# Performance work log

Hardware: AMD Instinct MI355X
Metric: run time of the kernel (lower is better)

Reference implementation:

```python
import jax, jax.numpy as jnp
import numpy as np

NSTEPS = 4
STEPSIZE = 1.0
B, N_PATCHES, D_LAT = 4, 81920, 32
HIDDEN, D_DYN = 128, 16


def setup_inputs() -> dict:
    key = jax.random.key(0)
    k1, k2, k3, k4 = jax.random.split(key, 4)
    z_old = jax.random.normal(k1, (B, N_PATCHES, D_LAT), dtype=jnp.float32)
    neighbour_list = jax.random.randint(k2, (N_PATCHES, 3), 0, N_PATCHES, dtype=jnp.int32)
    W1 = jax.random.normal(k3, (4 * D_LAT, HIDDEN), dtype=jnp.float32) * (1.0 / np.sqrt(4 * D_LAT))
    b1 = jnp.zeros((HIDDEN,), dtype=jnp.float32)
    W2 = jax.random.normal(k4, (HIDDEN, D_DYN), dtype=jnp.float32) * (1.0 / np.sqrt(HIDDEN))
    b2 = jnp.zeros((D_DYN,), dtype=jnp.float32)
    return {"z_old": z_old, "neighbour_list": neighbour_list, "W1": W1, "b1": b1, "W2": W2, "b2": b2}


def _step(z, neighbour_list, W1, b1, W2, b2):
    # gather neighbour features: (B, n_patches, 3, d_lat)
    neigh = z[:, neighbour_list, :]
    # z_mid: (B, n_patches, d_lat, 4) with slot 0 = self, slots 1..3 = neighbours
    z_mid = jnp.concatenate([z[..., None], jnp.swapaxes(neigh, -1, -2)], axis=-1)
    flat = z_mid.reshape(z.shape[0], z.shape[1], -1)  # (B, n_patches, 4*d_lat)
    h = jnp.tanh(flat @ W1 + b1)
    F_theta = h @ W2 + b2  # (B, n_patches, d_dyn)
    return z.at[:, :, :F_theta.shape[-1]].add(STEPSIZE * F_theta)


def reference(z_old, neighbour_list, W1, b1, W2, b2):
    z = z_old
    for _ in range(NSTEPS):
        z = _step(z, neighbour_list, W1, b1, W2, b2)
    return z
```

## Files before the change

### kernel.cpp

```cpp
#include <hip/hip_runtime.h>
#include <hip/hip_bf16.h>

typedef unsigned short u16;
typedef unsigned int u32;
typedef __attribute__((ext_vector_type(8))) short bf16x8;
typedef __attribute__((ext_vector_type(4))) float f32x4;
typedef __attribute__((ext_vector_type(4))) u16 u16x4;

#define NPATCH 81920
#define NBATCH 4
#define NROWS (NBATCH * NPATCH)
#define HID 128
#define CHUNK 64
#define NCHUNK (NROWS / CHUNK)
#define CPB (NPATCH / CHUNK)
#define GSTRIDE 512

__device__ __forceinline__ u16 f2bf(float x) {
  union { __hip_bfloat16 b; u16 u; } c; c.b = __float2bfloat16(x); return c.u;
}
__device__ __forceinline__ float bf2f(u16 h) {
  union { __hip_bfloat16 b; u16 u; } c; c.u = h; return __bfloat162float(c.b);
}

#define GLD(g, l) __builtin_amdgcn_global_load_lds( \
    (const __attribute__((address_space(1))) void*)(g), \
    (__attribute__((address_space(3))) void*)(l), 16, 0, 0)
#define SBAR() __builtin_amdgcn_s_barrier()
#define SCHED0() __builtin_amdgcn_sched_barrier(0)

__global__ void prep_w(const float* __restrict__ W1, const float* __restrict__ W2,
                       u16* __restrict__ wf, u16* __restrict__ w2f) {
  int t = blockIdx.x * 256 + threadIdx.x;
  if (t < 128 * 128) {
    int kp = t >> 7, n = t & 127;
    int s = kp >> 5, d = kp & 31;
    float v = W1[(d * 4 + s) * HID + n];
    u16 h = f2bf(v);
    u16 l = f2bf(v - bf2f(h));
    int kg = kp >> 3, j = kp & 7;
    int o = (kg * 128 + n) * 8 + j;
    wf[o] = h;
    wf[16384 + o] = l;
  } else if (t < 128 * 128 + 2048) {
    int u = t - 128 * 128;
    int k = u >> 4, o = u & 15;
    float v = W2[k * 16 + o];
    u16 h = f2bf(v);
    u16 l = f2bf(v - bf2f(h));
    int kt = k >> 5, lg = (k >> 3) & 3, j = k & 7;
    int idx = ((kt * 4 + lg) * 16 + o) * 8 + j;
    w2f[idx] = h;
    w2f[2048 + idx] = l;
  }
}

template<int MERGED>
__global__ void prep_z(const float* __restrict__ z, u16* __restrict__ A0, u16* __restrict__ B0) {
  int t = blockIdx.x * 256 + threadIdx.x;
  if (t >= NROWS * 8) return;
  size_t row = (size_t)(t >> 3);
  int q = t & 7;
  float4 v = *(const float4*)&z[row * 32 + q * 4];
  u16 h0 = f2bf(v.x), h1 = f2bf(v.y), h2 = f2bf(v.z), h3 = f2bf(v.w);
  u16 l0 = f2bf(v.x - bf2f(h0)), l1 = f2bf(v.y - bf2f(h1));
  u16 l2 = f2bf(v.z - bf2f(h2)), l3 = f2bf(v.w - bf2f(h3));
  u16x4 hh = {h0, h1, h2, h3};
  u16x4 ll = {l0, l1, l2, l3};
  int dd = (q & 3) * 4;
  if (MERGED) {
    int reg = (q < 4) ? 0 : 32;
    *(u16x4*)&A0[row * 64 + reg + dd] = hh;
    *(u16x4*)&A0[row * 64 + reg + 16 + dd] = ll;
    *(u16x4*)&B0[row * 64 + reg + dd] = hh;
    *(u16x4*)&B0[row * 64 + reg + 16 + dd] = ll;
  } else {
    u16* buf = (q < 4) ? A0 : B0;
    *(u16x4*)&buf[row * 32 + dd] = hh;
    *(u16x4*)&buf[row * 32 + 16 + dd] = ll;
  }
}

template<int FIRST, int LAST, int MERGED>
__global__ __launch_bounds__(256, 2) void step_kernel(
    const u16* __restrict__ Zin, u16* __restrict__ Zout,
    const u16* __restrict__ Sst,
    const float* __restrict__ zold, float* __restrict__ zf,
    const int* __restrict__ nl, const float* __restrict__ b1,
    const float* __restrict__ b2, const u16* __restrict__ wf,
    const u16* __restrict__ w2f) {
  __shared__ __align__(16) u16 AH[2][16 * 64 * 8];
  __shared__ __align__(16) u16 AL[2][16 * 64 * 8];
  __shared__ __align__(16) u16 W2H[2048];
  __shared__ __align__(16) u16 W2L[2048];

  const int tid = threadIdx.x;
  const int lane = tid & 63;
  const int w = tid >> 6;
  const int li = lane & 15;
  const int lg = lane >> 4;

  #pragma unroll
  for (int c = 0; c < 2; ++c) {
    int idx = tid + c * 256;
    int part = idx >> 8, slot = idx & 255;
    u16* dst = part ? W2L : W2H;
    *(bf16x8*)&dst[slot * 8] = *(const bf16x8*)&w2f[part * 2048 + slot * 8];
  }

  bf16x8 WH[2][4], WL[2][4];
  #pragma unroll
  for (int nt = 0; nt < 2; ++nt)
    #pragma unroll
    for (int kt = 0; kt < 4; ++kt) {
      int kg = kt * 4 + lg;
      int n = w * 32 + nt * 16 + li;
      WH[nt][kt] = *(const bf16x8*)&wf[(kg * 128 + n) * 8];
      WL[nt][kt] = *(const bf16x8*)&wf[16384 + (kg * 128 + n) * 8];
    }

  float b1v[2][4];
  #pragma unroll
  for (int nt = 0; nt < 2; ++nt)
    #pragma unroll
    for (int r = 0; r < 4; ++r)
      b1v[nt][r] = b1[w * 32 + nt * 16 + lg * 4 + r];
  float b2v = b2[li];

  #define NVLOAD(CN) nl[(((CN) * CHUNK - ((CN) / CPB) * NPATCH) + lane) * 3 + (w - 1)]

  #define STAGE(BUF, CN, NV) do {                                          \
    int b_ = (CN) / CPB;                                                   \
    int pb_ = (CN) * CHUNK - b_ * NPATCH;                                  \
    int ps_ = w ? (NV) : (pb_ + lane);                                     \
    size_t r_ = (size_t)b_ * NPATCH + (size_t)ps_;                         \
    u16* ah_ = &AH[BUF][(w * 4) * 512];                                    \
    u16* al_ = &AL[BUF][(w * 4) * 512];                                    \
    if (MERGED) {                                                          \
      const u16* s_ = Zin + r_ * 64;                                       \
      GLD(s_ + 0,  ah_ + 0);    GLD(s_ + 8,  ah_ + 512);                   \
      GLD(s_ + 32, ah_ + 1024); GLD(s_ + 40, ah_ + 1536);                  \
      GLD(s_ + 16, al_ + 0);    GLD(s_ + 24, al_ + 512);                   \
      GLD(s_ + 48, al_ + 1024); GLD(s_ + 56, al_ + 1536);                  \
    } else {                                                               \
      const u16* d_ = Zin + r_ * 32;                                       \
      const u16* t_ = Sst + r_ * 32;                                       \
      GLD(d_ + 0,  ah_ + 0);    GLD(d_ + 8,  ah_ + 512);                   \
      GLD(t_ + 0,  ah_ + 1024); GLD(t_ + 8,  ah_ + 1536);                  \
      GLD(d_ + 16, al_ + 0);    GLD(d_ + 24, al_ + 512);                   \
      GLD(t_ + 16, al_ + 1024); GLD(t_ + 24, al_ + 1536);                  \
    }                                                                      \
  } while (0)

  int c0 = blockIdx.x;
  int nv = 0, nv1 = 0;
  if (w) nv = NVLOAD(c0);
  {
    int c1 = c0 + GSTRIDE; if (c1 > NCHUNK - 1) c1 = NCHUNK - 1;
    if (w) nv1 = NVLOAD(c1);
  }
  STAGE(0, c0, nv);
  asm volatile("s_waitcnt lgkmcnt(0)" ::: "memory");
  int cur = 0;

  for (int c = c0; c < NCHUNK; c += GSTRIDE) {
    int cn = c + GSTRIDE;
    bool hn = cn < NCHUNK;
    if (hn) STAGE(cur ^ 1, cn, nv1);
    {
      int cnn = cn + GSTRIDE; if (cnn > NCHUNK - 1) cnn = NCHUNK - 1;
      if (w && hn) nv1 = NVLOAD(cnn);
    }
    if (!hn)        { asm volatile("s_waitcnt vmcnt(0)" ::: "memory"); }
    else if (w == 0){ asm volatile("s_waitcnt vmcnt(8)" ::: "memory"); }
    else            { asm volatile("s_waitcnt vmcnt(9)" ::: "memory"); }
    SCHED0(); SBAR(); SCHED0();

    f32x4 acc[2][4];
    #pragma unroll
    for (int nt = 0; nt < 2; ++nt)
      #pragma unroll
      for (int mt = 0; mt < 4; ++mt)
        acc[nt][mt] = (f32x4){0.f, 0.f, 0.f, 0.f};

    #pragma unroll
    for (int kt = 0; kt < 4; ++kt) {
      #pragma unroll
      for (int mt = 0; mt < 4; ++mt) {
        int off = ((kt * 4 + lg) * 64 + mt * 16 + li) * 8;
        bf16x8 ah = *(const bf16x8*)&AH[cur][off];
        bf16x8 al = *(const bf16x8*)&AL[cur][off];
        #pragma unroll
        for (int nt = 0; nt < 2; ++nt) {
          acc[nt][mt] = __builtin_amdgcn_mfma_f32_16x16x32_bf16(WH[nt][kt], ah, acc[nt][mt], 0, 0, 0);
          acc[nt][mt] = __builtin_amdgcn_mfma_f32_16x16x32_bf16(WH[nt][kt], al, acc[nt][mt], 0, 0, 0);
          acc[nt][mt] = __builtin_amdgcn_mfma_f32_16x16x32_bf16(WL[nt][kt], ah, acc[nt][mt], 0, 0, 0);
        }
      }
    }
    SCHED0(); SBAR(); SCHED0();

    #pragma unroll
    for (int nt = 0; nt < 2; ++nt) {
      #pragma unroll
      for (int mt = 0; mt < 4; ++mt) {
        u16 hh[4], ll[4];
        #pragma unroll
        for (int r = 0; r < 4; ++r) {
          float hval = acc[nt][mt][r] + b1v[nt][r];
          float e = __expf(2.0f * hval);
          float t = 1.0f - 2.0f / (e + 1.0f);
          hh[r] = f2bf(t);
          ll[r] = f2bf(t - bf2f(hh[r]));
        }
        int base = ((w * 4 + nt * 2 + (lg >> 1)) * 64 + mt * 16 + li) * 8 + (lg & 1) * 4;
        u16x4 hv = {hh[0], hh[1], hh[2], hh[3]};
        u16x4 lv = {ll[0], ll[1], ll[2], ll[3]};
        *(u16x4*)&AH[cur][base] = hv;
        *(u16x4*)&AL[cur][base] = lv;
      }
    }
    asm volatile("s_waitcnt lgkmcnt(0)" ::: "memory");
    SCHED0(); SBAR(); SCHED0();

    f32x4 acc2 = (f32x4){0.f, 0.f, 0.f, 0.f};
    #pragma unroll
    for (int kt = 0; kt < 4; ++kt) {
      int woff = ((kt * 4 + lg) * 16 + li) * 8;
      bf16x8 wh = *(const bf16x8*)&W2H[woff];
      bf16x8 wl = *(const bf16x8*)&W2L[woff];
      int off = ((kt * 4 + lg) * 64 + w * 16 + li) * 8;
      bf16x8 hh = *(const bf16x8*)&AH[cur][off];
      bf16x8 hl = *(const bf16x8*)&AL[cur][off];
      acc2 = __builtin_amdgcn_mfma_f32_16x16x32_bf16(hh, wh, acc2, 0, 0, 0);
      acc2 = __builtin_amdgcn_mfma_f32_16x16x32_bf16(hl, wh, acc2, 0, 0, 0);
      acc2 = __builtin_amdgcn_mfma_f32_16x16x32_bf16(hh, wl, acc2, 0, 0, 0);
    }

    #pragma unroll
    for (int r = 0; r < 4; ++r) {
      int rowg = c * CHUNK + w * 16 + lg * 4 + r;
      float F = acc2[r] + b2v;
      float zi = FIRST ? zold[(size_t)rowg * 32 + li] : zf[(size_t)rowg * 32 + li];
      float v = zi + F;
      zf[(size_t)rowg * 32 + li] = v;
      if (LAST) {
        zf[(size_t)rowg * 32 + 16 + li] = zold[(size_t)rowg * 32 + 16 + li];
      } else {
        u16 h = f2bf(v);
        u16 l = f2bf(v - bf2f(h));
        if (MERGED) {
          Zout[(size_t)rowg * 64 + li] = h;
          Zout[(size_t)rowg * 64 + 16 + li] = l;
        } else {
          Zout[(size_t)rowg * 32 + li] = h;
          Zout[(size_t)rowg * 32 + 16 + li] = l;
        }
      }
    }
    cur ^= 1;
  }
  #undef STAGE
  #undef NVLOAD
}

extern "C" void kernel_launch(void* const* d_in, const int* in_sizes, int n_in,
                              void* d_out, int out_size, void* d_ws, size_t ws_size,
                              hipStream_t stream) {
  const float* z_old = (const float*)d_in[0];
  const int* nl = (const int*)d_in[1];
  const float* W1 = (const float*)d_in[2];
  const float* b1 = (const float*)d_in[3];
  const float* W2 = (const float*)d_in[4];
  const float* b2 = (const float*)d_in[5];
  float* out = (float*)d_out;

  const size_t wOff = 73728;
  const size_t DbM = (size_t)NROWS * 64 * sizeof(u16);
  const size_t DbS = (size_t)NROWS * 32 * sizeof(u16);
  const size_t needM = wOff + 2 * DbM;
  u16* wf = (u16*)d_ws;
  u16* w2f = wf + 32768;
  char* base = (char*)d_ws + wOff;

  prep_w<<<72, 256, 0, stream>>>(W1, W2, wf, w2f);

  if (ws_size >= needM) {
    u16* ZA = (u16*)base;
    u16* ZB = (u16*)(base + DbM);
    prep_z<1><<<(NROWS * 8) / 256, 256, 0, stream>>>(z_old, ZA, ZB);
    step_kernel<1, 0, 1><<<GSTRIDE, 256, 0, stream>>>(ZA, ZB, nullptr, z_old, out, nl, b1, b2, wf, w2f);
    step_kernel<0, 0, 1><<<GSTRIDE, 256, 0, stream>>>(ZB, ZA, nullptr, z_old, out, nl, b1, b2, wf, w2f);
    step_kernel<0, 0, 1><<<GSTRIDE, 256, 0, stream>>>(ZA, ZB, nullptr, z_old, out, nl, b1, b2, wf, w2f);
    step_kernel<0, 1, 1><<<GSTRIDE, 256, 0, stream>>>(ZB, ZA, nullptr, z_old, out, nl, b1, b2, wf, w2f);
  } else {
    u16* S  = (u16*)base;
    u16* DA = (u16*)(base + DbS);
    u16* DB = (u16*)(base + 2 * DbS);
    prep_z<0><<<(NROWS * 8) / 256, 256, 0, stream>>>(z_old, DA, S);
    step_kernel<1, 0, 0><<<GSTRIDE, 256, 0, stream>>>(DA, DB, S, z_old, out, nl, b1, b2, wf, w2f);
    step_kernel<0, 0, 0><<<GSTRIDE, 256, 0, stream>>>(DB, DA, S, z_old, out, nl, b1, b2, wf, w2f);
    step_kernel<0, 0, 0><<<GSTRIDE, 256, 0, stream>>>(DA, DB, S, z_old, out, nl, b1, b2, wf, w2f);
    step_kernel<0, 1, 0><<<GSTRIDE, 256, 0, stream>>>(DB, DA, S, z_old, out, nl, b1, b2, wf, w2f);
  }
}
```

Before: 362.3 us.

## Restructure step kernel to per-wave 32-row tiles with register-held activations

Each wave now independently processes 32 rows, gathering neighbour rows directly into registers instead of staging them through LDS with global_load_lds and block barriers. W1 (hi/lo bf16 split) is cached in LDS and read per MFMA, while the hidden activations are moved between MFMA layouts with ds_bpermute instead of an LDS round trip. Stores and the residual load become 16-byte vectorised, and the tanh division becomes a hardware reciprocal. This removes block-level syncs, but it adds register pressure (acc[8][2], prefetched A fragments), many bpermute ops, and W1 LDS reads in every iteration.

```diff
diff --git a/kernel.cpp b/kernel.cpp
--- a/kernel.cpp
+++ b/kernel.cpp
@@ -6,15 +6,14 @@
 typedef __attribute__((ext_vector_type(8))) short bf16x8;
 typedef __attribute__((ext_vector_type(4))) float f32x4;
 typedef __attribute__((ext_vector_type(4))) u16 u16x4;
+typedef __attribute__((ext_vector_type(4))) u32 u32x4;
 
 #define NPATCH 81920
 #define NBATCH 4
 #define NROWS (NBATCH * NPATCH)
 #define HID 128
-#define CHUNK 64
-#define NCHUNK (NROWS / CHUNK)
-#define CPB (NPATCH / CHUNK)
-#define GSTRIDE 512
+#define NC32 (NROWS / 32)
+#define GRID 512
 
 __device__ __forceinline__ u16 f2bf(float x) {
   union { __hip_bfloat16 b; u16 u; } c; c.b = __float2bfloat16(x); return c.u;
@@ -23,11 +22,7 @@
   union { __hip_bfloat16 b; u16 u; } c; c.u = h; return __bfloat162float(c.b);
 }
 
-#define GLD(g, l) __builtin_amdgcn_global_load_lds( \
-    (const __attribute__((address_space(1))) void*)(g), \
-    (__attribute__((address_space(3))) void*)(l), 16, 0, 0)
-#define SBAR() __builtin_amdgcn_s_barrier()
-#define SCHED0() __builtin_amdgcn_sched_barrier(0)
+union B8 { u32x4 u; bf16x8 b; };
 
 __global__ void prep_w(const float* __restrict__ W1, const float* __restrict__ W2,
                        u16* __restrict__ wf, u16* __restrict__ w2f) {
@@ -89,10 +84,7 @@
     const int* __restrict__ nl, const float* __restrict__ b1,
     const float* __restrict__ b2, const u16* __restrict__ wf,
     const u16* __restrict__ w2f) {
-  __shared__ __align__(16) u16 AH[2][16 * 64 * 8];
-  __shared__ __align__(16) u16 AL[2][16 * 64 * 8];
-  __shared__ __align__(16) u16 W2H[2048];
-  __shared__ __align__(16) u16 W2L[2048];
+  __shared__ __align__(16) u16 W1L[32768];
 
   const int tid = threadIdx.x;
   const int lane = tid & 63;
@@ -101,167 +93,215 @@
   const int lg = lane >> 4;
 
   #pragma unroll
-  for (int c = 0; c < 2; ++c) {
-    int idx = tid + c * 256;
-    int part = idx >> 8, slot = idx & 255;
-    u16* dst = part ? W2L : W2H;
-    *(bf16x8*)&dst[slot * 8] = *(const bf16x8*)&w2f[part * 2048 + slot * 8];
-  }
-
-  bf16x8 WH[2][4], WL[2][4];
-  #pragma unroll
-  for (int nt = 0; nt < 2; ++nt)
+  for (int i = 0; i < 16; ++i)
+    *(bf16x8*)&W1L[i * 2048 + tid * 8] = *(const bf16x8*)&wf[i * 2048 + tid * 8];
+  __syncthreads();
+
+  const int wid = blockIdx.x * 4 + w;
+  const int soff = lg * 8 + ((lg >> 1) << 4);
+  const int a0 = (li + ((lg & 1) << 5)) << 2;
+  const int a1 = a0 + 64;
+  const f32x4 b2v = *(const f32x4*)&b2[lg * 4];
+
+  int nlv[3][2], nlv2[3][2];
+  bf16x8 ah[4][2], al[4][2];
+
+  #define LOADNL(CC, DST) do {                                              \
+    int r0_ = (CC) * 32;                                                    \
+    int b_ = r0_ / NPATCH;                                                  \
+    int pb_ = r0_ - b_ * NPATCH;                                            \
+    _Pragma("unroll")                                                       \
+    for (int mt_ = 0; mt_ < 2; ++mt_) {                                     \
+      int p_ = pb_ + mt_ * 16 + li;                                         \
+      DST[0][mt_] = nl[p_ * 3 + 0];                                         \
+      DST[1][mt_] = nl[p_ * 3 + 1];                                         \
+      DST[2][mt_] = nl[p_ * 3 + 2];                                         \
+    }                                                                       \
+  } while (0)
+
+  #define LOADA(CC, NV) do {                                                \
+    int r0_ = (CC) * 32;                                                    \
+    int b_ = r0_ / NPATCH;                                                  \
+    int pb_ = r0_ - b_ * NPATCH;                                            \
+    size_t rb_ = (size_t)b_ * NPATCH;                                       \
+    _Pragma("unroll")                                                       \
+    for (int mt_ = 0; mt_ < 2; ++mt_) {                                     \
+      int self_ = pb_ + mt_ * 16 + li;                                      \
+      _Pragma("unroll")                                                     \
+      for (int kt_ = 0; kt_ < 4; ++kt_) {                                   \
+        int ps_ = (kt_ == 0) ? self_ : NV[kt_ - 1][mt_];                    \
+        if (MERGED) {                                                       \
+          const u16* p_ = Zin + (rb_ + (size_t)ps_) * 64 + soff;            \
+          ah[kt_][mt_] = *(const bf16x8*)p_;                                \
+          al[kt_][mt_] = *(const bf16x8*)(p_ + 16);                         \
+        } else {                                                            \
+          const u16* base_ = (lg < 2) ? (Zin + (rb_ + (size_t)ps_) * 32)    \
+                                      : (Sst + (rb_ + (size_t)ps_) * 32);   \
+          const u16* p_ = base_ + (lg & 1) * 8;                             \
+          ah[kt_][mt_] = *(const bf16x8*)p_;                                \
+          al[kt_][mt_] = *(const bf16x8*)(p_ + 16);                         \
+        }                                                                   \
+      }                                                                     \
+    }                                                                       \
+  } while (0)
+
+  if (wid >= NC32) return;
+  LOADNL(wid, nlv);
+  LOADA(wid, nlv);
+  {
+    int c1 = wid + GRID * 4; if (c1 > NC32 - 1) c1 = NC32 - 1;
+    LOADNL(c1, nlv2);
+  }
+
+  for (int c = wid; c < NC32; c += GRID * 4) {
+    const int cn = c + GRID * 4;
+    const bool hn = cn < NC32;
+
+    f32x4 zi[2], zs[2];
+    #pragma unroll
+    for (int mt = 0; mt < 2; ++mt) {
+      int rowg = c * 32 + mt * 16 + li;
+      zi[mt] = FIRST ? *(const f32x4*)&zold[(size_t)rowg * 32 + lg * 4]
+                     : *(const f32x4*)&zf[(size_t)rowg * 32 + lg * 4];
+      if (LAST) zs[mt] = *(const f32x4*)&zold[(size_t)rowg * 32 + 16 + lg * 4];
+    }
+
+    f32x4 acc[8][2];
+    #pragma unroll
+    for (int nt = 0; nt < 8; ++nt)
+      #pragma unroll
+      for (int mt = 0; mt < 2; ++mt)
+        acc[nt][mt] = (f32x4){0.f, 0.f, 0.f, 0.f};
+
     #pragma unroll
     for (int kt = 0; kt < 4; ++kt) {
-      int kg = kt * 4 + lg;
-      int n = w * 32 + nt * 16 + li;
-      WH[nt][kt] = *(const bf16x8*)&wf[(kg * 128 + n) * 8];
-      WL[nt][kt] = *(const bf16x8*)&wf[16384 + (kg * 128 + n) * 8];
-    }
-
-  float b1v[2][4];
-  #pragma unroll
-  for (int nt = 0; nt < 2; ++nt)
-    #pragma unroll
-    for (int r = 0; r < 4; ++r)
-      b1v[nt][r] = b1[w * 32 + nt * 16 + lg * 4 + r];
-  float b2v = b2[li];
-
-  #define NVLOAD(CN) nl[(((CN) * CHUNK - ((CN) / CPB) * NPATCH) + lane) * 3 + (w - 1)]
-
-  #define STAGE(BUF, CN, NV) do {                                          \
-    int b_ = (CN) / CPB;                                                   \
-    int pb_ = (CN) * CHUNK - b_ * NPATCH;                                  \
-    int ps_ = w ? (NV) : (pb_ + lane);                                     \
-    size_t r_ = (size_t)b_ * NPATCH + (size_t)ps_;                         \
-    u16* ah_ = &AH[BUF][(w * 4) * 512];                                    \
-    u16* al_ = &AL[BUF][(w * 4) * 512];                                    \
-    if (MERGED) {                                                          \
-      const u16* s_ = Zin + r_ * 64;                                       \
-      GLD(s_ + 0,  ah_ + 0);    GLD(s_ + 8,  ah_ + 512);                   \
-      GLD(s_ + 32, ah_ + 1024); GLD(s_ + 40, ah_ + 1536);                  \
-      GLD(s_ + 16, al_ + 0);    GLD(s_ + 24, al_ + 512);                   \
-      GLD(s_ + 48, al_ + 1024); GLD(s_ + 56, al_ + 1536);                  \
-    } else {                                                               \
-      const u16* d_ = Zin + r_ * 32;                                       \
-      const u16* t_ = Sst + r_ * 32;                                       \
-      GLD(d_ + 0,  ah_ + 0);    GLD(d_ + 8,  ah_ + 512);                   \
-      GLD(t_ + 0,  ah_ + 1024); GLD(t_ + 8,  ah_ + 1536);                  \
-      GLD(d_ + 16, al_ + 0);    GLD(d_ + 24, al_ + 512);                   \
-      GLD(t_ + 16, al_ + 1024); GLD(t_ + 24, al_ + 1536);                  \
-    }                                                                      \
-  } while (0)
-
-  int c0 = blockIdx.x;
-  int nv = 0, nv1 = 0;
-  if (w) nv = NVLOAD(c0);
-  {
-    int c1 = c0 + GSTRIDE; if (c1 > NCHUNK - 1) c1 = NCHUNK - 1;
-    if (w) nv1 = NVLOAD(c1);
-  }
-  STAGE(0, c0, nv);
-  asm volatile("s_waitcnt lgkmcnt(0)" ::: "memory");
-  int cur = 0;
-
-  for (int c = c0; c < NCHUNK; c += GSTRIDE) {
-    int cn = c + GSTRIDE;
-    bool hn = cn < NCHUNK;
-    if (hn) STAGE(cur ^ 1, cn, nv1);
-    {
-      int cnn = cn + GSTRIDE; if (cnn > NCHUNK - 1) cnn = NCHUNK - 1;
-      if (w && hn) nv1 = NVLOAD(cnn);
-    }
-    if (!hn)        { asm volatile("s_waitcnt vmcnt(0)" ::: "memory"); }
-    else if (w == 0){ asm volatile("s_waitcnt vmcnt(8)" ::: "memory"); }
-    else            { asm volatile("s_waitcnt vmcnt(9)" ::: "memory"); }
-    SCHED0(); SBAR(); SCHED0();
-
-    f32x4 acc[2][4];
-    #pragma unroll
-    for (int nt = 0; nt < 2; ++nt)
-      #pragma unroll
-      for (int mt = 0; mt < 4; ++mt)
-        acc[nt][mt] = (f32x4){0.f, 0.f, 0.f, 0.f};
-
-    #pragma unroll
-    for (int kt = 0; kt < 4; ++kt) {
-      #pragma unroll
-      for (int mt = 0; mt < 4; ++mt) {
-        int off = ((kt * 4 + lg) * 64 + mt * 16 + li) * 8;
-        bf16x8 ah = *(const bf16x8*)&AH[cur][off];
-        bf16x8 al = *(const bf16x8*)&AL[cur][off];
+      #pragma unroll
+      for (int nt = 0; nt < 8; ++nt) {
+        int woff = ((kt * 4 + lg) * 128 + nt * 16 + li) * 8;
+        bf16x8 whf = *(const bf16x8*)&W1L[woff];
+        bf16x8 wlf = *(const bf16x8*)&W1L[16384 + woff];
         #pragma unroll
-        for (int nt = 0; nt < 2; ++nt) {
-          acc[nt][mt] = __builtin_amdgcn_mfma_f32_16x16x32_bf16(WH[nt][kt], ah, acc[nt][mt], 0, 0, 0);
-          acc[nt][mt] = __builtin_amdgcn_mfma_f32_16x16x32_bf16(WH[nt][kt], al, acc[nt][mt], 0, 0, 0);
-          acc[nt][mt] = __builtin_amdgcn_mfma_f32_16x16x32_bf16(WL[nt][kt], ah, acc[nt][mt], 0, 0, 0);
+        for (int mt = 0; mt < 2; ++mt) {
+          acc[nt][mt] = __builtin_amdgcn_mfma_f32_16x16x32_bf16(whf, ah[kt][mt], acc[nt][mt], 0, 0, 0);
+          acc[nt][mt] = __builtin_amdgcn_mfma_f32_16x16x32_bf16(whf, al[kt][mt], acc[nt][mt], 0, 0, 0);
+          acc[nt][mt] = __builtin_amdgcn_mfma_f32_16x16x32_bf16(wlf, ah[kt][mt], acc[nt][mt], 0, 0, 0);
         }
       }
     }
-    SCHED0(); SBAR(); SCHED0();
-
-    #pragma unroll
-    for (int nt = 0; nt < 2; ++nt) {
-      #pragma unroll
-      for (int mt = 0; mt < 4; ++mt) {
-        u16 hh[4], ll[4];
+
+    u32 H01[2][8], H23[2][8], L01[2][8], L23[2][8];
+    #pragma unroll
+    for (int nt = 0; nt < 8; ++nt) {
+      f32x4 bb = *(const f32x4*)&b1[nt * 16 + lg * 4];
+      #pragma unroll
+      for (int mt = 0; mt < 2; ++mt) {
+        u16 hu[4]; float lo[4];
         #pragma unroll
         for (int r = 0; r < 4; ++r) {
-          float hval = acc[nt][mt][r] + b1v[nt][r];
-          float e = __expf(2.0f * hval);
-          float t = 1.0f - 2.0f / (e + 1.0f);
-          hh[r] = f2bf(t);
-          ll[r] = f2bf(t - bf2f(hh[r]));
+          float x = acc[nt][mt][r] + bb[r];
+          float e = __expf(2.0f * x);
+          float t = 1.0f - 2.0f * __builtin_amdgcn_rcpf(e + 1.0f);
+          u16 h = f2bf(t);
+          hu[r] = h;
+          lo[r] = t - bf2f(h);
         }
-        int base = ((w * 4 + nt * 2 + (lg >> 1)) * 64 + mt * 16 + li) * 8 + (lg & 1) * 4;
-        u16x4 hv = {hh[0], hh[1], hh[2], hh[3]};
-        u16x4 lv = {ll[0], ll[1], ll[2], ll[3]};
-        *(u16x4*)&AH[cur][base] = hv;
-        *(u16x4*)&AL[cur][base] = lv;
+        H01[mt][nt] = (u32)hu[0] | ((u32)hu[1] << 16);
+        H23[mt][nt] = (u32)hu[2] | ((u32)hu[3] << 16);
+        L01[mt][nt] = (u32)f2bf(lo[0]) | ((u32)f2bf(lo[1]) << 16);
+        L23[mt][nt] = (u32)f2bf(lo[2]) | ((u32)f2bf(lo[3]) << 16);
       }
     }
-    asm volatile("s_waitcnt lgkmcnt(0)" ::: "memory");
-    SCHED0(); SBAR(); SCHED0();
-
-    f32x4 acc2 = (f32x4){0.f, 0.f, 0.f, 0.f};
-    #pragma unroll
-    for (int kt = 0; kt < 4; ++kt) {
-      int woff = ((kt * 4 + lg) * 16 + li) * 8;
-      bf16x8 wh = *(const bf16x8*)&W2H[woff];
-      bf16x8 wl = *(const bf16x8*)&W2L[woff];
-      int off = ((kt * 4 + lg) * 64 + w * 16 + li) * 8;
-      bf16x8 hh = *(const bf16x8*)&AH[cur][off];
-      bf16x8 hl = *(const bf16x8*)&AL[cur][off];
-      acc2 = __builtin_amdgcn_mfma_f32_16x16x32_bf16(hh, wh, acc2, 0, 0, 0);
-      acc2 = __builtin_amdgcn_mfma_f32_16x16x32_bf16(hl, wh, acc2, 0, 0, 0);
-      acc2 = __builtin_amdgcn_mfma_f32_16x16x32_bf16(hh, wl, acc2, 0, 0, 0);
-    }
-
-    #pragma unroll
-    for (int r = 0; r < 4; ++r) {
-      int rowg = c * CHUNK + w * 16 + lg * 4 + r;
-      float F = acc2[r] + b2v;
-      float zi = FIRST ? zold[(size_t)rowg * 32 + li] : zf[(size_t)rowg * 32 + li];
-      float v = zi + F;
-      zf[(size_t)rowg * 32 + li] = v;
+
+    if (hn) LOADA(cn, nlv2);
+
+    bf16x8 w2h[4], w2l[4];
+    #pragma unroll
+    for (int s = 0; s < 4; ++s) {
+      int o = ((s * 4 + lg) * 16 + li) * 8;
+      w2h[s] = *(const bf16x8*)&w2f[o];
+      w2l[s] = *(const bf16x8*)&w2f[2048 + o];
+    }
+
+    const bool odd = (lg >= 2);
+    f32x4 acc2[2];
+    #pragma unroll
+    for (int mt = 0; mt < 2; ++mt) {
+      acc2[mt] = (f32x4){0.f, 0.f, 0.f, 0.f};
+      #pragma unroll
+      for (int s = 0; s < 4; ++s) {
+        B8 hf, lf;
+        u32 e0, e1;
+        e0 = (u32)__builtin_amdgcn_ds_bpermute(a0, (int)H01[mt][2 * s]);
+        e1 = (u32)__builtin_amdgcn_ds_bpermute(a0, (int)H01[mt][2 * s + 1]);
+        hf.u[0] = odd ? e1 : e0;
+        e0 = (u32)__builtin_amdgcn_ds_bpermute(a0, (int)H23[mt][2 * s]);
+        e1 = (u32)__builtin_amdgcn_ds_bpermute(a0, (int)H23[mt][2 * s + 1]);
+        hf.u[1] = odd ? e1 : e0;
+        e0 = (u32)__builtin_amdgcn_ds_bpermute(a1, (int)H01[mt][2 * s]);
+        e1 = (u32)__builtin_amdgcn_ds_bpermute(a1, (int)H01[mt][2 * s + 1]);
+        hf.u[2] = odd ? e1 : e0;
+        e0 = (u32)__builtin_amdgcn_ds_bpermute(a1, (int)H23[mt][2 * s]);
+        e1 = (u32)__builtin_amdgcn_ds_bpermute(a1, (int)H23[mt][2 * s + 1]);
+        hf.u[3] = odd ? e1 : e0;
+
+        e0 = (u32)__builtin_amdgcn_ds_bpermute(a0, (int)L01[mt][2 * s]);
+        e1 = (u32)__builtin_amdgcn_ds_bpermute(a0, (int)L01[mt][2 * s + 1]);
+        lf.u[0] = odd ? e1 : e0;
+        e0 = (u32)__builtin_amdgcn_ds_bpermute(a0, (int)L23[mt][2 * s]);
+        e1 = (u32)__builtin_amdgcn_ds_bpermute(a0, (int)L23[mt][2 * s + 1]);
+        lf.u[1] = odd ? e1 : e0;
+        e0 = (u32)__builtin_amdgcn_ds_bpermute(a1, (int)L01[mt][2 * s]);
+        e1 = (u32)__builtin_amdgcn_ds_bpermute(a1, (int)L01[mt][2 * s + 1]);
+        lf.u[2] = odd ? e1 : e0;
+        e0 = (u32)__builtin_amdgcn_ds_bpermute(a1, (int)L23[mt][2 * s]);
+        e1 = (u32)__builtin_amdgcn_ds_bpermute(a1, (int)L23[mt][2 * s + 1]);
+        lf.u[3] = odd ? e1 : e0;
+
+        acc2[mt] = __builtin_amdgcn_mfma_f32_16x16x32_bf16(w2h[s], hf.b, acc2[mt], 0, 0, 0);
+        acc2[mt] = __builtin_amdgcn_mfma_f32_16x16x32_bf16(w2h[s], lf.b, acc2[mt], 0, 0, 0);
+        acc2[mt] = __builtin_amdgcn_mfma_f32_16x16x32_bf16(w2l[s], hf.b, acc2[mt], 0, 0, 0);
+      }
+    }
+
+    #pragma unroll
+    for (int mt = 0; mt < 2; ++mt) {
+      int rowg = c * 32 + mt * 16 + li;
+      f32x4 v;
+      #pragma unroll
+      for (int r = 0; r < 4; ++r) v[r] = zi[mt][r] + acc2[mt][r] + b2v[r];
+      *(f32x4*)&zf[(size_t)rowg * 32 + lg * 4] = v;
       if (LAST) {
-        zf[(size_t)rowg * 32 + 16 + li] = zold[(size_t)rowg * 32 + 16 + li];
+        *(f32x4*)&zf[(size_t)rowg * 32 + 16 + lg * 4] = zs[mt];
       } else {
-        u16 h = f2bf(v);
-        u16 l = f2bf(v - bf2f(h));
+        u16x4 hv, lv;
+        #pragma unroll
+        for (int r = 0; r < 4; ++r) {
+          u16 h = f2bf(v[r]);
+          hv[r] = h;
+          lv[r] = f2bf(v[r] - bf2f(h));
+        }
         if (MERGED) {
-          Zout[(size_t)rowg * 64 + li] = h;
-          Zout[(size_t)rowg * 64 + 16 + li] = l;
+          *(u16x4*)&Zout[(size_t)rowg * 64 + lg * 4] = hv;
+          *(u16x4*)&Zout[(size_t)rowg * 64 + 16 + lg * 4] = lv;
         } else {
-          Zout[(size_t)rowg * 32 + li] = h;
-          Zout[(size_t)rowg * 32 + 16 + li] = l;
+          *(u16x4*)&Zout[(size_t)rowg * 32 + lg * 4] = hv;
+          *(u16x4*)&Zout[(size_t)rowg * 32 + 16 + lg * 4] = lv;
         }
       }
     }
-    cur ^= 1;
-  }
-  #undef STAGE
-  #undef NVLOAD
+
+    #pragma unroll
+    for (int k = 0; k < 3; ++k)
+      #pragma unroll
+      for (int mt = 0; mt < 2; ++mt)
+        nlv[k][mt] = nlv2[k][mt];
+    {
+      int c2 = cn + GRID * 4; if (c2 > NC32 - 1) c2 = NC32 - 1;
+      if (hn) LOADNL(c2, nlv2);
+    }
+  }
+  #undef LOADA
+  #undef LOADNL
 }
 
 extern "C" void kernel_launch(void* const* d_in, const int* in_sizes, int n_in,
@@ -289,18 +329,18 @@
     u16* ZA = (u16*)base;
     u16* ZB = (u16*)(base + DbM);
     prep_z<1><<<(NROWS * 8) / 256, 256, 0, stream>>>(z_old, ZA, ZB);
-    step_kernel<1, 0, 1><<<GSTRIDE, 256, 0, stream>>>(ZA, ZB, nullptr, z_old, out, nl, b1, b2, wf, w2f);
-    step_kernel<0, 0, 1><<<GSTRIDE, 256, 0, stream>>>(ZB, ZA, nullptr, z_old, out, nl, b1, b2, wf, w2f);
-    step_kernel<0, 0, 1><<<GSTRIDE, 256, 0, stream>>>(ZA, ZB, nullptr, z_old, out, nl, b1, b2, wf, w2f);
-    step_kernel<0, 1, 1><<<GSTRIDE, 256, 0, stream>>>(ZB, ZA, nullptr, z_old, out, nl, b1, b2, wf, w2f);
+    step_kernel<1, 0, 1><<<GRID, 256, 0, stream>>>(ZA, ZB, nullptr, z_old, out, nl, b1, b2, wf, w2f);
+    step_kernel<0, 0, 1><<<GRID, 256, 0, stream>>>(ZB, ZA, nullptr, z_old, out, nl, b1, b2, wf, w2f);
+    step_kernel<0, 0, 1><<<GRID, 256, 0, stream>>>(ZA, ZB, nullptr, z_old, out, nl, b1, b2, wf, w2f);
+    step_kernel<0, 1, 1><<<GRID, 256, 0, stream>>>(ZB, ZA, nullptr, z_old, out, nl, b1, b2, wf, w2f);
   } else {
     u16* S  = (u16*)base;
     u16* DA = (u16*)(base + DbS);
     u16* DB = (u16*)(base + 2 * DbS);
     prep_z<0><<<(NROWS * 8) / 256, 256, 0, stream>>>(z_old, DA, S);
-    step_kernel<1, 0, 0><<<GSTRIDE, 256, 0, stream>>>(DA, DB, S, z_old, out, nl, b1, b2, wf, w2f);
-    step_kernel<0, 0, 0><<<GSTRIDE, 256, 0, stream>>>(DB, DA, S, z_old, out, nl, b1, b2, wf, w2f);
-    step_kernel<0, 0, 0><<<GSTRIDE, 256, 0, stream>>>(DA, DB, S, z_old, out, nl, b1, b2, wf, w2f);
-    step_kernel<0, 1, 0><<<GSTRIDE, 256, 0, stream>>>(DB, DA, S, z_old, out, nl, b1, b2, wf, w2f);
-  }
-}
+    step_kernel<1, 0, 0><<<GRID, 256, 0, stream>>>(DA, DB, S, z_old, out, nl, b1, b2, wf, w2f);
+    step_kernel<0, 0, 0><<<GRID, 256, 0, stream>>>(DB, DA, S, z_old, out, nl, b1, b2, wf, w2f);
+    step_kernel<0, 0, 0><<<GRID, 256, 0, stream>>>(DA, DB, S, z_old, out, nl, b1, b2, wf, w2f);
+    step_kernel<0, 1, 0><<<GRID, 256, 0, stream>>>(DB, DA, S, z_old, out, nl, b1, b2, wf, w2f);
+  }
+}
```

Result: slower. 775.4 us (+114.0%).

## Drop LDS double buffering, keep W2 in registers, raise occupancy to five blocks

Applied to the files above, without the earlier changes.

Removes the double-buffered LDS staging pipeline in favor of a single buffer with a trailing barrier. W2 fragments move from shared memory into registers. LDS per block drops, so the launch bound rises to 5 blocks per CU and the grid grows from 512 to 1280 blocks, relying on more resident waves to hide gather latency instead of software prefetch. Tanh now uses a hardware reciprocal, which may lose a little precision, and the higher occupancy target may force register spills.

```diff
diff --git a/kernel.cpp b/kernel.cpp
--- a/kernel.cpp
+++ b/kernel.cpp
@@ -14,7 +14,7 @@
 #define CHUNK 64
 #define NCHUNK (NROWS / CHUNK)
 #define CPB (NPATCH / CHUNK)
-#define GSTRIDE 512
+#define GRID 1280
 
 __device__ __forceinline__ u16 f2bf(float x) {
   union { __hip_bfloat16 b; u16 u; } c; c.b = __float2bfloat16(x); return c.u;
@@ -82,17 +82,15 @@
 }
 
 template<int FIRST, int LAST, int MERGED>
-__global__ __launch_bounds__(256, 2) void step_kernel(
+__global__ __launch_bounds__(256, 5) void step_kernel(
     const u16* __restrict__ Zin, u16* __restrict__ Zout,
     const u16* __restrict__ Sst,
     const float* __restrict__ zold, float* __restrict__ zf,
     const int* __restrict__ nl, const float* __restrict__ b1,
     const float* __restrict__ b2, const u16* __restrict__ wf,
     const u16* __restrict__ w2f) {
-  __shared__ __align__(16) u16 AH[2][16 * 64 * 8];
-  __shared__ __align__(16) u16 AL[2][16 * 64 * 8];
-  __shared__ __align__(16) u16 W2H[2048];
-  __shared__ __align__(16) u16 W2L[2048];
+  __shared__ __align__(16) u16 AH[16 * 64 * 8];
+  __shared__ __align__(16) u16 AL[16 * 64 * 8];
 
   const int tid = threadIdx.x;
   const int lane = tid & 63;
@@ -100,14 +98,6 @@
   const int li = lane & 15;
   const int lg = lane >> 4;
 
-  #pragma unroll
-  for (int c = 0; c < 2; ++c) {
-    int idx = tid + c * 256;
-    int part = idx >> 8, slot = idx & 255;
-    u16* dst = part ? W2L : W2H;
-    *(bf16x8*)&dst[slot * 8] = *(const bf16x8*)&w2f[part * 2048 + slot * 8];
-  }
-
   bf16x8 WH[2][4], WL[2][4];
   #pragma unroll
   for (int nt = 0; nt < 2; ++nt)
@@ -118,6 +108,13 @@
       WH[nt][kt] = *(const bf16x8*)&wf[(kg * 128 + n) * 8];
       WL[nt][kt] = *(const bf16x8*)&wf[16384 + (kg * 128 + n) * 8];
     }
+  bf16x8 w2h[4], w2l[4];
+  #pragma unroll
+  for (int kt = 0; kt < 4; ++kt) {
+    int o = ((kt * 4 + lg) * 16 + li) * 8;
+    w2h[kt] = *(const bf16x8*)&w2f[o];
+    w2l[kt] = *(const bf16x8*)&w2f[2048 + o];
+  }
 
   float b1v[2][4];
   #pragma unroll
@@ -129,13 +126,13 @@
 
   #define NVLOAD(CN) nl[(((CN) * CHUNK - ((CN) / CPB) * NPATCH) + lane) * 3 + (w - 1)]
 
-  #define STAGE(BUF, CN, NV) do {                                          \
+  #define STAGE(CN, NV) do {                                               \
     int b_ = (CN) / CPB;                                                   \
     int pb_ = (CN) * CHUNK - b_ * NPATCH;                                  \
     int ps_ = w ? (NV) : (pb_ + lane);                                     \
     size_t r_ = (size_t)b_ * NPATCH + (size_t)ps_;                         \
-    u16* ah_ = &AH[BUF][(w * 4) * 512];                                    \
-    u16* al_ = &AL[BUF][(w * 4) * 512];                                    \
+    u16* ah_ = &AH[(w * 4) * 512];                                         \
+    u16* al_ = &AL[(w * 4) * 512];                                         \
     if (MERGED) {                                                          \
       const u16* s_ = Zin + r_ * 64;                                       \
       GLD(s_ + 0,  ah_ + 0);    GLD(s_ + 8,  ah_ + 512);                   \
@@ -153,27 +150,17 @@
   } while (0)
 
   int c0 = blockIdx.x;
-  int nv = 0, nv1 = 0;
+  int nv = 0;
   if (w) nv = NVLOAD(c0);
-  {
-    int c1 = c0 + GSTRIDE; if (c1 > NCHUNK - 1) c1 = NCHUNK - 1;
-    if (w) nv1 = NVLOAD(c1);
-  }
-  STAGE(0, c0, nv);
-  asm volatile("s_waitcnt lgkmcnt(0)" ::: "memory");
-  int cur = 0;
-
-  for (int c = c0; c < NCHUNK; c += GSTRIDE) {
-    int cn = c + GSTRIDE;
-    bool hn = cn < NCHUNK;
-    if (hn) STAGE(cur ^ 1, cn, nv1);
+
+  for (int c = c0; c < NCHUNK; c += GRID) {
+    STAGE(c, nv);
     {
-      int cnn = cn + GSTRIDE; if (cnn > NCHUNK - 1) cnn = NCHUNK - 1;
-      if (w && hn) nv1 = NVLOAD(cnn);
-    }
-    if (!hn)        { asm volatile("s_waitcnt vmcnt(0)" ::: "memory"); }
-    else if (w == 0){ asm volatile("s_waitcnt vmcnt(8)" ::: "memory"); }
-    else            { asm volatile("s_waitcnt vmcnt(9)" ::: "memory"); }
+      int cn = c + GRID; if (cn > NCHUNK - 1) cn = NCHUNK - 1;
+      if (w) nv = NVLOAD(cn);
+    }
+    if (w) { asm volatile("s_waitcnt vmcnt(1)" ::: "memory"); }
+    else   { asm volatile("s_waitcnt vmcnt(0)" ::: "memory"); }
     SCHED0(); SBAR(); SCHED0();
 
     f32x4 acc[2][4];
@@ -188,8 +175,8 @@
       #pragma unroll
       for (int mt = 0; mt < 4; ++mt) {
         int off = ((kt * 4 + lg) * 64 + mt * 16 + li) * 8;
-        bf16x8 ah = *(const bf16x8*)&AH[cur][off];
-        bf16x8 al = *(const bf16x8*)&AL[cur][off];
+        bf16x8 ah = *(const bf16x8*)&AH[off];
+        bf16x8 al = *(const bf16x8*)&AL[off];
         #pragma unroll
         for (int nt = 0; nt < 2; ++nt) {
           acc[nt][mt] = __builtin_amdgcn_mfma_f32_16x16x32_bf16(WH[nt][kt], ah, acc[nt][mt], 0, 0, 0);
@@ -209,15 +196,15 @@
         for (int r = 0; r < 4; ++r) {
           float hval = acc[nt][mt][r] + b1v[nt][r];
           float e = __expf(2.0f * hval);
-          float t = 1.0f - 2.0f / (e + 1.0f);
+          float t = 1.0f - 2.0f * __builtin_amdgcn_rcpf(e + 1.0f);
           hh[r] = f2bf(t);
           ll[r] = f2bf(t - bf2f(hh[r]));
         }
         int base = ((w * 4 + nt * 2 + (lg >> 1)) * 64 + mt * 16 + li) * 8 + (lg & 1) * 4;
         u16x4 hv = {hh[0], hh[1], hh[2], hh[3]};
         u16x4 lv = {ll[0], ll[1], ll[2], ll[3]};
-        *(u16x4*)&AH[cur][base] = hv;
-        *(u16x4*)&AL[cur][base] = lv;
+        *(u16x4*)&AH[base] = hv;
+        *(u16x4*)&AL[base] = lv;
       }
     }
     asm volatile("s_waitcnt lgkmcnt(0)" ::: "memory");
@@ -226,15 +213,12 @@
     f32x4 acc2 = (f32x4){0.f, 0.f, 0.f, 0.f};
     #pragma unroll
     for (int kt = 0; kt < 4; ++kt) {
-      int woff = ((kt * 4 + lg) * 16 + li) * 8;
-      bf16x8 wh = *(const bf16x8*)&W2H[woff];
-      bf16x8 wl = *(const bf16x8*)&W2L[woff];
       int off = ((kt * 4 + lg) * 64 + w * 16 + li) * 8;
-      bf16x8 hh = *(const bf16x8*)&AH[cur][off];
-      bf16x8 hl = *(const bf16x8*)&AL[cur][off];
-      acc2 = __builtin_amdgcn_mfma_f32_16x16x32_bf16(hh, wh, acc2, 0, 0, 0);
-      acc2 = __builtin_amdgcn_mfma_f32_16x16x32_bf16(hl, wh, acc2, 0, 0, 0);
-      acc2 = __builtin_amdgcn_mfma_f32_16x16x32_bf16(hh, wl, acc2, 0, 0, 0);
+      bf16x8 hh = *(const bf16x8*)&AH[off];
+      bf16x8 hl = *(const bf16x8*)&AL[off];
+      acc2 = __builtin_amdgcn_mfma_f32_16x16x32_bf16(hh, w2h[kt], acc2, 0, 0, 0);
+      acc2 = __builtin_amdgcn_mfma_f32_16x16x32_bf16(hl, w2h[kt], acc2, 0, 0, 0);
+      acc2 = __builtin_amdgcn_mfma_f32_16x16x32_bf16(hh, w2l[kt], acc2, 0, 0, 0);
     }
 
     #pragma unroll
@@ -258,7 +242,7 @@
         }
       }
     }
-    cur ^= 1;
+    SCHED0(); SBAR(); SCHED0();
   }
   #undef STAGE
   #undef NVLOAD
@@ -289,18 +273,18 @@
     u16* ZA = (u16*)base;
     u16* ZB = (u16*)(base + DbM);
     prep_z<1><<<(NROWS * 8) / 256, 256, 0, stream>>>(z_old, ZA, ZB);
-    step_kernel<1, 0, 1><<<GSTRIDE, 256, 0, stream>>>(ZA, ZB, nullptr, z_old, out, nl, b1, b2, wf, w2f);
-    step_kernel<0, 0, 1><<<GSTRIDE, 256, 0, stream>>>(ZB, ZA, nullptr, z_old, out, nl, b1, b2, wf, w2f);
-    step_kernel<0, 0, 1><<<GSTRIDE, 256, 0, stream>>>(ZA, ZB, nullptr, z_old, out, nl, b1, b2, wf, w2f);
-    step_kernel<0, 1, 1><<<GSTRIDE, 256, 0, stream>>>(ZB, ZA, nullptr, z_old, out, nl, b1, b2, wf, w2f);
+    step_kernel<1, 0, 1><<<GRID, 256, 0, stream>>>(ZA, ZB, nullptr, z_old, out, nl, b1, b2, wf, w2f);
+    step_kernel<0, 0, 1><<<GRID, 256, 0, stream>>>(ZB, ZA, nullptr, z_old, out, nl, b1, b2, wf, w2f);
+    step_kernel<0, 0, 1><<<GRID, 256, 0, stream>>>(ZA, ZB, nullptr, z_old, out, nl, b1, b2, wf, w2f);
+    step_kernel<0, 1, 1><<<GRID, 256, 0, stream>>>(ZB, ZA, nullptr, z_old, out, nl, b1, b2, wf, w2f);
   } else {
     u16* S  = (u16*)base;
     u16* DA = (u16*)(base + DbS);
     u16* DB = (u16*)(base + 2 * DbS);
     prep_z<0><<<(NROWS * 8) / 256, 256, 0, stream>>>(z_old, DA, S);
-    step_kernel<1, 0, 0><<<GSTRIDE, 256, 0, stream>>>(DA, DB, S, z_old, out, nl, b1, b2, wf, w2f);
-    step_kernel<0, 0, 0><<<GSTRIDE, 256, 0, stream>>>(DB, DA, S, z_old, out, nl, b1, b2, wf, w2f);
-    step_kernel<0, 0, 0><<<GSTRIDE, 256, 0, stream>>>(DA, DB, S, z_old, out, nl, b1, b2, wf, w2f);
-    step_kernel<0, 1, 0><<<GSTRIDE, 256, 0, stream>>>(DB, DA, S, z_old, out, nl, b1, b2, wf, w2f);
-  }
-}
+    step_kernel<1, 0, 0><<<GRID, 256, 0, stream>>>(DA, DB, S, z_old, out, nl, b1, b2, wf, w2f);
+    step_kernel<0, 0, 0><<<GRID, 256, 0, stream>>>(DB, DA, S, z_old, out, nl, b1, b2, wf, w2f);
+    step_kernel<0, 0, 0><<<GRID, 256, 0, stream>>>(DA, DB, S, z_old, out, nl, b1, b2, wf, w2f);
+    step_kernel<0, 1, 0><<<GRID, 256, 0, stream>>>(DB, DA, S, z_old, out, nl, b1, b2, wf, w2f);
+  }
+}
```

New measurement: 689.2 us. +90.2%, slower.
